# Kernel tuning notes

Hardware: AMD Instinct MI355X
Metric: run time of the kernel (lower is better)

The kernel has to match this reference:

```python
import jax, jax.numpy as jnp
import numpy as np

NH = 8  # num_heads


def _conv1x1(w, b, x):
    # 1x1 conv == channel matmul: w [O,C], x [B,C,H,W]
    return jnp.einsum('oc,bchw->bohw', w, x) + b[None, :, None, None]


def _fwd(low_freq_feat, high_freq_feat, ext_context, road_feat,
         ext_proj_w, ext_proj_b, road_proj_w, road_proj_b,
         ext_qkv_w, ext_qkv_b, road_qkv_w, road_qkv_b,
         ext_out_w, ext_out_b, road_out_w, road_out_b,
         gate_ext_w, gate_ext_b, gate_road_w, gate_road_b):
    B, C, H, W = low_freq_feat.shape
    nh = NH
    hd = C // nh
    HW = H * W
    scale = hd ** -0.5

    ext_p = ext_context @ ext_proj_w.T + ext_proj_b          # [B,C]
    road_p = _conv1x1(road_proj_w, road_proj_b, road_feat)   # [B,C,H,W]

    eqkv = (ext_p @ ext_qkv_w.T + ext_qkv_b).reshape(B, 3, nh, hd)
    ext_q, ext_v = eqkv[:, 0], eqkv[:, 2]                    # [B,nh,hd]

    # torch: conv out [B,3C,H,W] viewed as (B,C,3,H,W) -> q/k/v interleaved over channels
    rqkv = _conv1x1(road_qkv_w, road_qkv_b, road_p).reshape(B, C, 3, H, W)
    road_k = rqkv[:, :, 1].reshape(B, nh, hd, HW).transpose(0, 1, 3, 2)  # [B,nh,HW,hd]
    road_v = rqkv[:, :, 2].reshape(B, nh, hd, HW).transpose(0, 1, 3, 2)

    # ext->road attention. The torch code expands ext_q to HW identical rows; one row
    # per (batch, head) gives a bit-identical result without the [B,nh,HW,HW] blowup.
    scores = jnp.einsum('bnd,bnpd->bnp', ext_q, road_k) * scale
    attn = jax.nn.softmax(scores, axis=-1)                   # [B,nh,HW]
    ext_head = jnp.einsum('bnp,bnpd->bnd', attn, road_v).reshape(B, C)
    ext_vec = ext_head @ ext_out_w.T + ext_out_b             # [B,C]
    ext_feat_spatial = jnp.broadcast_to(ext_vec[:, :, None, None], (B, C, H, W))

    # road->ext attention: all HW keys/values are copies of the single ext token, so
    # softmax is exactly uniform and the output per position is exactly ext_v. The
    # road_out 1x1 conv on a spatially-constant map is a single matvec per batch.
    road_vec = ext_v.reshape(B, C) @ road_out_w.T + road_out_b
    road_enhanced = jnp.broadcast_to(road_vec[:, :, None, None], (B, C, H, W))

    # gated fusion (ext stream): spatial mean of constant map == ext_vec
    gate_in = jnp.concatenate([low_freq_feat.mean(axis=(2, 3)), ext_vec], axis=-1)
    ext_gate = jax.nn.sigmoid(gate_in @ gate_ext_w.T + gate_ext_b)[:, :, None, None]
    ext_final = low_freq_feat * (1.0 - ext_gate) + ext_feat_spatial * ext_gate

    # gated fusion (road stream)
    rg_in = jnp.concatenate([high_freq_feat, road_enhanced], axis=1)  # [B,2C,H,W]
    road_gate = jax.nn.sigmoid(_conv1x1(gate_road_w, gate_road_b, rg_in))
    road_final = high_freq_feat * (1.0 - road_gate) + road_enhanced * road_gate
    return ext_final, road_final


def setup_inputs() -> dict:
    key = jax.random.key(0)
    ks = jax.random.split(key, 20)
    B, C, H, W, E = 8, 256, 64, 64, 64
    f = lambda k, shape, s=1.0: jax.random.normal(k, shape, dtype=jnp.float32) * s
    return {
        'low_freq_feat': f(ks[0], (B, C, H, W)),
        'high_freq_feat': f(ks[1], (B, C, H, W)),
        'ext_context': f(ks[2], (B, E)),
        'road_feat': f(ks[3], (B, C, H, W)),
        'ext_proj_w': f(ks[4], (C, E), 0.05), 'ext_proj_b': f(ks[5], (C,), 0.02),
        'road_proj_w': f(ks[6], (C, C), 0.05), 'road_proj_b': f(ks[7], (C,), 0.02),
        'ext_qkv_w': f(ks[8], (3 * C, C), 0.05), 'ext_qkv_b': f(ks[9], (3 * C,), 0.02),
        'road_qkv_w': f(ks[10], (3 * C, C), 0.05), 'road_qkv_b': f(ks[11], (3 * C,), 0.02),
        'ext_out_w': f(ks[12], (C, C), 0.05), 'ext_out_b': f(ks[13], (C,), 0.02),
        'road_out_w': f(ks[14], (C, C), 0.05), 'road_out_b': f(ks[15], (C,), 0.02),
        'gate_ext_w': f(ks[16], (C, 2 * C), 0.05), 'gate_ext_b': f(ks[17], (C,), 0.02),
        'gate_road_w': f(ks[18], (C, 2 * C), 0.05), 'gate_road_b': f(ks[19], (C,), 0.02),
    }


def reference(low_freq_feat, high_freq_feat, ext_context, road_feat,
              ext_proj_w, ext_proj_b, road_proj_w, road_proj_b,
              ext_qkv_w, ext_qkv_b, road_qkv_w, road_qkv_b,
              ext_out_w, ext_out_b, road_out_w, road_out_b,
              gate_ext_w, gate_ext_b, gate_road_w, gate_road_b):
    return _fwd(low_freq_feat, high_freq_feat, ext_context, road_feat,
                ext_proj_w, ext_proj_b, road_proj_w, road_proj_b,
                ext_qkv_w, ext_qkv_b, road_qkv_w, road_qkv_b,
                ext_out_w, ext_out_b, road_out_w, road_out_b,
                gate_ext_w, gate_ext_b, gate_road_w, gate_road_b)
```

## Files before the change

### kernel.cpp

```cpp
#include <hip/hip_runtime.h>

typedef short bf16x8 __attribute__((ext_vector_type(8)));
typedef float f32x4 __attribute__((ext_vector_type(4)));

__device__ __forceinline__ unsigned short f2b(float f) {
    unsigned int u = __builtin_bit_cast(unsigned int, f);
    unsigned int r = u + 0x7FFFu + ((u >> 16) & 1u);
    return (unsigned short)(r >> 16);
}
__device__ __forceinline__ float wsum64(float v) {
    #pragma unroll
    for (int m = 32; m; m >>= 1) v += __shfl_xor(v, m, 64);
    return v;
}


__global__ __launch_bounds__(256) void k_setup(const float* __restrict__ w1,
                                               const float* __restrict__ wqkv,
                                               const float* __restrict__ b1,
                                               const float* __restrict__ bqkv,
                                               const float* __restrict__ gate_road_w,
                                               const float* __restrict__ ext_proj_w,
                                               const float* __restrict__ ext_qkv_w,
                                               const float* __restrict__ road_out_w,
                                               const float* __restrict__ ext_out_w,
                                               const float* __restrict__ gate_ext_w,
                                               const float* __restrict__ low,
                                               unsigned short* __restrict__ W3b,
                                               unsigned short* __restrict__ Wcb,
                                               unsigned short* __restrict__ WF,
                                               float* __restrict__ bcv,
                                               float* __restrict__ mean_low) {
    int bid = blockIdx.x, t = threadIdx.x;
    __shared__ float sel[8][256];
    __shared__ float red[8][4];
    if (bid >= 448) {
        int bc = bid - 448;
        const f32x4* p4 = (const f32x4*)(low + (size_t)bc * 4096);
        float s = 0.f;
        for (int i = t; i < 1024; i += 256) {
            f32x4 v = p4[i];
            s += v[0] + v[1] + v[2] + v[3];
        }
        s = wsum64(s);
        if ((t & 63) == 0) red[0][t >> 6] = s;
        __syncthreads();
        if (t == 0) mean_low[bc] = (red[0][0] + red[0][1] + red[0][2] + red[0][3]) * (1.0f / 4096.0f);
    } else if (bid < 256) {
        int i = bid * 256 + t;
        int o = i >> 8, k = i & 255;
        W3b[i] = f2b(gate_road_w[o * 512 + k]);
    } else if (bid < 320) {
        int o0 = (bid - 256) * 8;
        #pragma unroll
        for (int r = 0; r < 8; r++) {
            int o = o0 + r;
            int c = (o < 256) ? o : o - 256;
            int g = (o < 256) ? 1 : 2;
            sel[r][t] = wqkv[(size_t)(3 * c + g) * 256 + t];
        }
        __syncthreads();
        float b1v = b1[t];
        #pragma unroll
        for (int r = 0; r < 8; r++) {
            float v = wsum64(sel[r][t] * b1v);
            if ((t & 63) == 0) red[r][t >> 6] = v;
        }
        __syncthreads();
        if (t < 8) {
            int o = o0 + t;
            int c = (o < 256) ? o : o - 256;
            int g = (o < 256) ? 1 : 2;
            bcv[o] = red[t][0] + red[t][1] + red[t][2] + red[t][3] + bqkv[3 * c + g];
        }
        float acc[8] = {};
        #pragma unroll 16
        for (int m = 0; m < 256; m++) {
            float w1v = w1[(size_t)m * 256 + t];
            #pragma unroll
            for (int r = 0; r < 8; r++) acc[r] += sel[r][m] * w1v;
        }
        #pragma unroll
        for (int r = 0; r < 8; r++) Wcb[(size_t)(o0 + r) * 256 + t] = f2b(acc[r]);
    } else {
        int mb = bid - 320;
        int m = mb >> 4, ctile = mb & 15;
        const float* src;
        int stride, K, coff;
        unsigned short* dst;
        switch (m) {
        case 0: src = ext_qkv_w;                     stride = 256; K = 256; coff = 0;   dst = WF;          break;
        case 1: src = ext_qkv_w + (size_t)512 * 256; stride = 256; K = 256; coff = 0;   dst = WF + 65536;  break;
        case 2: src = road_out_w;                    stride = 256; K = 256; coff = 0;   dst = WF + 131072; break;
        case 3: src = gate_road_w;                   stride = 512; K = 256; coff = 256; dst = WF + 196608; break;
        case 4: src = ext_proj_w;                    stride = 64;  K = 64;  coff = 0;   dst = WF + 262144; break;
        case 5: src = ext_out_w;                     stride = 256; K = 256; coff = 0;   dst = WF + 278528; break;
        case 6: src = gate_ext_w;                    stride = 512; K = 256; coff = 0;   dst = WF + 344064; break;
        default: src = gate_ext_w;                   stride = 512; K = 256; coff = 256; dst = WF + 409600; break;
        }
        int lc = t >> 4, kseg = t & 15;
        int k0 = kseg * 16;
        if (k0 < K) {
            int c = ctile * 16 + lc;
            const float* sp = src + (size_t)c * stride + coff + k0;
            f32x4 v0 = *(const f32x4*)sp;
            f32x4 v1 = *(const f32x4*)(sp + 4);
            f32x4 v2 = *(const f32x4*)(sp + 8);
            f32x4 v3 = *(const f32x4*)(sp + 12);
            int kk = kseg >> 1;
            int Kt = K >> 5;
            #pragma unroll
            for (int h = 0; h < 2; h++) {
                int lhi = (kseg & 1) * 2 + h;
                int lane = lhi * 16 + lc;
                bf16x8 o;
                f32x4 a = h ? v2 : v0, b = h ? v3 : v1;
                #pragma unroll
                for (int i = 0; i < 4; i++) { o[i] = (short)f2b(a[i]); o[4 + i] = (short)f2b(b[i]); }
                *(bf16x8*)(dst + ((size_t)(ctile * Kt + kk) << 9) + lane * 8) = o;
            }
        }
    }
}

__global__ __launch_bounds__(256) void k_tiny(const unsigned short* __restrict__ WF,
                                              const float* __restrict__ ext_context,
                                              const float* __restrict__ ext_proj_b,
                                              const float* __restrict__ ext_qkv_b,
                                              const float* __restrict__ road_out_b,
                                              const float* __restrict__ gate_road_b,
                                              float* __restrict__ ext_q,
                                              float* __restrict__ road_vec,
                                              float* __restrict__ rg_const) {
    __shared__ unsigned short xA[16][264];
    __shared__ unsigned short xB[16][264];
    int t = threadIdx.x;
    int w = t >> 6, lane = t & 63, l15 = lane & 15, lhi = lane >> 4;
    const unsigned short* WqF  = WF;
    const unsigned short* WvF  = WF + 65536;
    const unsigned short* WroF = WF + 131072;
    const unsigned short* WgF  = WF + 196608;
    const unsigned short* WpF  = WF + 262144;
    {
        int b = t >> 5, k0 = (t & 31) * 2;
        float c0v = ext_context[b * 64 + k0];
        float c1v = ext_context[b * 64 + k0 + 1];
        *(unsigned int*)&xA[b][k0] = (unsigned int)f2b(c0v) | ((unsigned int)f2b(c1v) << 16);
    }
    __syncthreads();
    {
        f32x4 acc[4] = {};
        #pragma unroll
        for (int kk = 0; kk < 2; kk++) {
            bf16x8 a = *(const bf16x8*)&xA[l15][kk * 32 + 8 * lhi];
            #pragma unroll
            for (int ni = 0; ni < 4; ni++) {
                int ct = w * 4 + ni;
                bf16x8 bfr = *(const bf16x8*)(WpF + ((size_t)(ct * 2 + kk) << 9) + lane * 8);
                acc[ni] = __builtin_amdgcn_mfma_f32_16x16x32_bf16(a, bfr, acc[ni], 0, 0, 0);
            }
        }
        if (lhi < 2) {
            #pragma unroll
            for (int ni = 0; ni < 4; ni++) {
                int c = w * 64 + ni * 16 + l15;
                float bp = ext_proj_b[c];
                #pragma unroll
                for (int r = 0; r < 4; r++)
                    xB[4 * lhi + r][c] = f2b(acc[ni][r] + bp);
            }
        }
    }
    __syncthreads();
    {
        f32x4 acc[8] = {};
        bool isq = (w < 2);
        int cbase = (w & 1) * 128;
        const unsigned short* Wb = isq ? WqF : WvF;
        for (int kk = 0; kk < 8; kk++) {
            bf16x8 a = *(const bf16x8*)&xB[l15][kk * 32 + 8 * lhi];
            #pragma unroll
            for (int ni = 0; ni < 8; ni++) {
                int ct = (cbase >> 4) + ni;
                bf16x8 bfr = *(const bf16x8*)(Wb + ((size_t)(ct * 8 + kk) << 9) + lane * 8);
                acc[ni] = __builtin_amdgcn_mfma_f32_16x16x32_bf16(a, bfr, acc[ni], 0, 0, 0);
            }
        }
        if (lhi < 2) {
            #pragma unroll
            for (int ni = 0; ni < 8; ni++) {
                int c = cbase + ni * 16 + l15;
                float bb = ext_qkv_b[(isq ? 0 : 512) + c];
                #pragma unroll
                for (int r = 0; r < 4; r++) {
                    int b = 4 * lhi + r;
                    float val = acc[ni][r] + bb;
                    if (isq) ext_q[b * 256 + c] = val;
                    else     xA[b][c] = f2b(val);
                }
            }
        }
    }
    __syncthreads();
    {
        f32x4 acc[4] = {};
        for (int kk = 0; kk < 8; kk++) {
            bf16x8 a = *(const bf16x8*)&xA[l15][kk * 32 + 8 * lhi];
            #pragma unroll
            for (int ni = 0; ni < 4; ni++) {
                int ct = w * 4 + ni;
                bf16x8 bfr = *(const bf16x8*)(WroF + ((size_t)(ct * 8 + kk) << 9) + lane * 8);
                acc[ni] = __builtin_amdgcn_mfma_f32_16x16x32_bf16(a, bfr, acc[ni], 0, 0, 0);
            }
        }
        if (lhi < 2) {
            #pragma unroll
            for (int ni = 0; ni < 4; ni++) {
                int c = w * 64 + ni * 16 + l15;
                float bb = road_out_b[c];
                #pragma unroll
                for (int r = 0; r < 4; r++) {
                    int b = 4 * lhi + r;
                    float val = acc[ni][r] + bb;
                    road_vec[b * 256 + c] = val;
                    xB[b][c] = f2b(val);
                }
            }
        }
    }
    __syncthreads();
    {
        f32x4 acc[4] = {};
        for (int kk = 0; kk < 8; kk++) {
            bf16x8 a = *(const bf16x8*)&xB[l15][kk * 32 + 8 * lhi];
            #pragma unroll
            for (int ni = 0; ni < 4; ni++) {
                int ct = w * 4 + ni;
                bf16x8 bfr = *(const bf16x8*)(WgF + ((size_t)(ct * 8 + kk) << 9) + lane * 8);
                acc[ni] = __builtin_amdgcn_mfma_f32_16x16x32_bf16(a, bfr, acc[ni], 0, 0, 0);
            }
        }
        if (lhi < 2) {
            #pragma unroll
            for (int ni = 0; ni < 4; ni++) {
                int c = w * 64 + ni * 16 + l15;
                float bb = gate_road_b[c];
                #pragma unroll
                for (int r = 0; r < 4; r++)
                    rg_const[(4 * lhi + r) * 256 + c] = acc[ni][r] + bb;
            }
        }
    }
}

__global__ __launch_bounds__(512) void k_kv(const float* __restrict__ road_feat,
                                            const unsigned short* __restrict__ Wcb,
                                            const float* __restrict__ bcv,
                                            const float* __restrict__ extq,
                                            float* __restrict__ part) {
    __shared__ unsigned short Xs[32 * 256];
    __shared__ float esh[8][32];
    char* Xc = (char*)Xs;
    int bid = ((blockIdx.x & 7) << 7) | (blockIdx.x >> 3);
    int b  = bid >> 7;
    int p0 = (bid & 127) << 5;
    int t  = threadIdx.x;
    const float* rfb = road_feat + (size_t)b * 1048576;

    int c0 = 2 * (t >> 3);
    int j4 = (t & 7) * 4;
    #pragma unroll
    for (int it = 0; it < 2; ++it) {
        int c = c0 + 128 * it;
        f32x4 g0 = *(const f32x4*)(rfb + (size_t)c * 4096 + p0 + j4);
        f32x4 g1 = *(const f32x4*)(rfb + (size_t)(c + 1) * 4096 + p0 + j4);
        #pragma unroll
        for (int i = 0; i < 4; i++) {
            int j = j4 + i;
            unsigned int pk = (unsigned int)f2b(g0[i]) | ((unsigned int)f2b(g1[i]) << 16);
            *(unsigned int*)(Xc + ((j * 512 + 2 * c) ^ ((j & 15) << 4))) = pk;
        }
    }
    __syncthreads();

    int w = t >> 6, lane = t & 63, l15 = lane & 15, lhi = lane >> 4;

    f32x4 acc[2][4] = {};
    for (int kk = 0; kk < 8; kk++) {
        bf16x8 a[2];
        #pragma unroll
        for (int mi = 0; mi < 2; mi++) {
            int j = mi * 16 + l15;
            int off = (j * 512 + (kk * 32 + 8 * lhi) * 2) ^ ((j & 15) << 4);
            a[mi] = *(const bf16x8*)((const char*)Xs + off);
        }
        #pragma unroll
        for (int ni = 0; ni < 4; ni++) {
            int n = w * 64 + ni * 16 + l15;
            bf16x8 bf = *(const bf16x8*)(Wcb + (size_t)n * 256 + kk * 32 + 8 * lhi);
            acc[0][ni] = __builtin_amdgcn_mfma_f32_16x16x32_bf16(a[0], bf, acc[0][ni], 0, 0, 0);
            acc[1][ni] = __builtin_amdgcn_mfma_f32_16x16x32_bf16(a[1], bf, acc[1][ni], 0, 0, 0);
        }
    }

    if (w < 4) {
        float qv[4], bk[4];
        #pragma unroll
        for (int ni = 0; ni < 4; ni++) {
            int n = w * 64 + ni * 16 + l15;
            qv[ni] = extq[b * 256 + n];
            bk[ni] = bcv[n];
        }
        #pragma unroll
        for (int mi = 0; mi < 2; mi++)
            #pragma unroll
            for (int r = 0; r < 4; r++) {
                int j = mi * 16 + 4 * lhi + r;
                #pragma unroll
                for (int hl = 0; hl < 2; hl++) {
                    float s = (acc[mi][2 * hl][r] + bk[2 * hl]) * qv[2 * hl]
                            + (acc[mi][2 * hl + 1][r] + bk[2 * hl + 1]) * qv[2 * hl + 1];
                    s += __shfl_xor(s, 1, 64);
                    s += __shfl_xor(s, 2, 64);
                    s += __shfl_xor(s, 4, 64);
                    s += __shfl_xor(s, 8, 64);
                    if (l15 == 0)
                        esh[w * 2 + hl][j] = expf(s * 0.17677669529663687f);
                }
            }
    }
    __syncthreads();

    float* pb = part + (size_t)bid * 264;
    if (w >= 4) {
        #pragma unroll
        for (int ni = 0; ni < 4; ni++) {
            int cv = (w - 4) * 64 + ni * 16 + l15;
            int hg = (w - 4) * 2 + (ni >> 1);
            float bv = bcv[256 + cv];
            float p = 0.f;
            #pragma unroll
            for (int mi = 0; mi < 2; mi++)
                #pragma unroll
                for (int r = 0; r < 4; r++) {
                    int j = mi * 16 + 4 * lhi + r;
                    p += esh[hg][j] * (acc[mi][ni][r] + bv);
                }
            p += __shfl_xor(p, 16, 64);
            p += __shfl_xor(p, 32, 64);
            if (lhi == 0) pb[8 + cv] = p;
        }
    } else {
        int h0 = w * 2;
        float v0 = (lane < 32) ? esh[h0][lane] : esh[h0 + 1][lane - 32];
        v0 += __shfl_xor(v0, 1, 64);
        v0 += __shfl_xor(v0, 2, 64);
        v0 += __shfl_xor(v0, 4, 64);
        v0 += __shfl_xor(v0, 8, 64);
        v0 += __shfl_xor(v0, 16, 64);
        if (lane == 0)  pb[h0] = v0;
        if (lane == 32) pb[h0 + 1] = v0;
    }
}

__global__ __launch_bounds__(256) void k_vec_combine(const float* __restrict__ part,
                                                     float* __restrict__ hdg) {
    int b = blockIdx.x, c = threadIdx.x;
    __shared__ float tot[8];
    const float* pb = part + (size_t)b * 128 * 264;
    float a = 0.f;
    #pragma unroll 8
    for (int tile = 0; tile < 128; tile++) a += pb[tile * 264 + 8 + c];
    if (c < 8) {
        float s = 0.f;
        #pragma unroll 8
        for (int tile = 0; tile < 128; tile++) s += pb[tile * 264 + c];
        tot[c] = 1.0f / s;
    }
    __syncthreads();
    hdg[b * 256 + c] = a * tot[c >> 5];
}

__global__ __launch_bounds__(256) void k_vec2(const unsigned short* __restrict__ WF,
                                              const float* __restrict__ hdg,
                                              const float* __restrict__ mean_low,
                                              const float* __restrict__ ext_out_b,
                                              const float* __restrict__ gate_ext_b,
                                              float* __restrict__ ext_vec,
                                              float* __restrict__ ext_gate) {
    __shared__ unsigned short xA[16][264];
    __shared__ unsigned short xB[16][264];
    __shared__ unsigned short xC[16][264];
    int t = threadIdx.x;
    int w = t >> 6, lane = t & 63, l15 = lane & 15, lhi = lane >> 4;
    const unsigned short* WoF    = WF + 278528;
    const unsigned short* WgeLoF = WF + 344064;
    const unsigned short* WgeHiF = WF + 409600;
    {
        int bb = t >> 5, kb = t & 31;
        #pragma unroll
        for (int q = 0; q < 4; q++) {
            int k0 = (kb + 32 * q) * 2;
            *(unsigned int*)&xA[bb][k0] =
                (unsigned int)f2b(hdg[bb * 256 + k0]) | ((unsigned int)f2b(hdg[bb * 256 + k0 + 1]) << 16);
            *(unsigned int*)&xB[bb][k0] =
                (unsigned int)f2b(mean_low[bb * 256 + k0]) | ((unsigned int)f2b(mean_low[bb * 256 + k0 + 1]) << 16);
        }
    }
    __syncthreads();
    {
        f32x4 acc[4] = {};
        for (int kk = 0; kk < 8; kk++) {
            bf16x8 a = *(const bf16x8*)&xA[l15][kk * 32 + 8 * lhi];
            #pragma unroll
            for (int ni = 0; ni < 4; ni++) {
                int ct = w * 4 + ni;
                bf16x8 bfr = *(const bf16x8*)(WoF + ((size_t)(ct * 8 + kk) << 9) + lane * 8);
                acc[ni] = __builtin_amdgcn_mfma_f32_16x16x32_bf16(a, bfr, acc[ni], 0, 0, 0);
            }
        }
        if (lhi < 2) {
            #pragma unroll
            for (int ni = 0; ni < 4; ni++) {
                int c = w * 64 + ni * 16 + l15;
                float bb = ext_out_b[c];
                #pragma unroll
                for (int r = 0; r < 4; r++) {
                    int b = 4 * lhi + r;
                    float val = acc[ni][r] + bb;
                    ext_vec[b * 256 + c] = val;
                    xC[b][c] = f2b(val);
                }
            }
        }
    }
    __syncthreads();
    {
        f32x4 acc[4] = {};
        for (int kk = 0; kk < 8; kk++) {
            bf16x8 a = *(const bf16x8*)&xB[l15][kk * 32 + 8 * lhi];
            #pragma unroll
            for (int ni = 0; ni < 4; ni++) {
                int ct = w * 4 + ni;
                bf16x8 bfr = *(const bf16x8*)(WgeLoF + ((size_t)(ct * 8 + kk) << 9) + lane * 8);
                acc[ni] = __builtin_amdgcn_mfma_f32_16x16x32_bf16(a, bfr, acc[ni], 0, 0, 0);
            }
        }
        for (int kk = 0; kk < 8; kk++) {
            bf16x8 a = *(const bf16x8*)&xC[l15][kk * 32 + 8 * lhi];
            #pragma unroll
            for (int ni = 0; ni < 4; ni++) {
                int ct = w * 4 + ni;
                bf16x8 bfr = *(const bf16x8*)(WgeHiF + ((size_t)(ct * 8 + kk) << 9) + lane * 8);
                acc[ni] = __builtin_amdgcn_mfma_f32_16x16x32_bf16(a, bfr, acc[ni], 0, 0, 0);
            }
        }
        if (lhi < 2) {
            #pragma unroll
            for (int ni = 0; ni < 4; ni++) {
                int c = w * 64 + ni * 16 + l15;
                float bb = gate_ext_b[c];
                #pragma unroll
                for (int r = 0; r < 4; r++) {
                    int b = 4 * lhi + r;
                    ext_gate[b * 256 + c] = 1.0f / (1.0f + expf(-(acc[ni][r] + bb)));
                }
            }
        }
    }
}

__global__ __launch_bounds__(256) void k_ext_final(const float* __restrict__ low,
                                                   const float* __restrict__ ext_vec,
                                                   const float* __restrict__ ext_gate,
                                                   float* __restrict__ out) {
    int idx = blockIdx.x * 256 + threadIdx.x;
    #pragma unroll
    for (int rep = 0; rep < 4; ++rep) {
        int i = idx + rep * 524288;
        int bc = i >> 10;
        float g = ext_gate[bc];
        float vv = ext_vec[bc];
        f32x4 L = *(const f32x4*)(low + (size_t)i * 4);
        f32x4 o;
        #pragma unroll
        for (int c = 0; c < 4; c++) o[c] = L[c] + g * (vv - L[c]);
        *(f32x4*)(out + (size_t)i * 4) = o;
    }
}

__global__ __launch_bounds__(512) void k_road(const float* __restrict__ high,
                                              const unsigned short* __restrict__ W3b,
                                              const float* __restrict__ rg_const,
                                              const float* __restrict__ road_vec,
                                              float* __restrict__ outbuf) {
    __shared__ float Xs[32 * 256];
    char* Xc = (char*)Xs;
    int bid = ((blockIdx.x & 7) << 7) | (blockIdx.x >> 3);
    int b  = bid >> 7;
    int p0 = (bid & 127) << 5;
    int t  = threadIdx.x;
    const float* hb = high + (size_t)b * 1048576;

    int c0 = t >> 3;
    int j4 = (t & 7) * 4;
    #pragma unroll
    for (int it = 0; it < 4; ++it) {
        int c = c0 + 64 * it;
        f32x4 g = *(const f32x4*)(hb + (size_t)c * 4096 + p0 + j4);
        #pragma unroll
        for (int i = 0; i < 4; i++) {
            int j = j4 + i;
            *(float*)(Xc + ((j * 1024 + 4 * c) ^ ((j & 15) << 4))) = g[i];
        }
    }
    __syncthreads();

    int w = t >> 6, lane = t & 63, l15 = lane & 15, lhi = lane >> 4;
    f32x4 acc[2][2] = {};
    for (int kk = 0; kk < 8; kk++) {
        bf16x8 a[2];
        #pragma unroll
        for (int mi = 0; mi < 2; mi++) {
            int j = mi * 16 + l15;
            int base = j * 1024 + (kk * 32 + 8 * lhi) * 4;
            int sw = (j & 15) << 4;
            f32x4 x0 = *(const f32x4*)(Xc + (base ^ sw));
            f32x4 x1 = *(const f32x4*)(Xc + ((base + 16) ^ sw));
            bf16x8 av;
            #pragma unroll
            for (int i = 0; i < 4; i++) {
                av[i]     = (short)f2b(x0[i]);
                av[4 + i] = (short)f2b(x1[i]);
            }
            a[mi] = av;
        }
        #pragma unroll
        for (int ni = 0; ni < 2; ni++) {
            int o = w * 32 + ni * 16 + l15;
            bf16x8 bf = *(const bf16x8*)(W3b + (size_t)o * 256 + kk * 32 + 8 * lhi);
            acc[0][ni] = __builtin_amdgcn_mfma_f32_16x16x32_bf16(a[0], bf, acc[0][ni], 0, 0, 0);
            acc[1][ni] = __builtin_amdgcn_mfma_f32_16x16x32_bf16(a[1], bf, acc[1][ni], 0, 0, 0);
        }
    }
    __syncthreads();

    #pragma unroll
    for (int ni = 0; ni < 2; ni++) {
        int o = w * 32 + ni * 16 + l15;
        float rc = rg_const[b * 256 + o];
        float rv = road_vec[b * 256 + o];
        #pragma unroll
        for (int mi = 0; mi < 2; mi++)
            #pragma unroll
            for (int r = 0; r < 4; r++) {
                int j = mi * 16 + 4 * lhi + r;
                float* slot = (float*)(Xc + ((j * 1024 + 4 * o) ^ ((j & 15) << 4)));
                float z = acc[mi][ni][r] + rc;
                float gte = 1.0f / (1.0f + expf(-z));
                float hv = *slot;
                *slot = hv + gte * (rv - hv);
            }
    }
    __syncthreads();

    float* ob = outbuf + 8388608 + (size_t)b * 1048576;
    #pragma unroll
    for (int it = 0; it < 4; ++it) {
        int c = c0 + 64 * it;
        f32x4 o4;
        #pragma unroll
        for (int i = 0; i < 4; i++) {
            int j = j4 + i;
            o4[i] = *(const float*)(Xc + ((j * 1024 + 4 * c) ^ ((j & 15) << 4)));
        }
        *(f32x4*)(ob + (size_t)c * 4096 + p0 + j4) = o4;
    }
}

extern "C" void kernel_launch(void* const* d_in, const int* in_sizes, int n_in,
                              void* d_out, int out_size, void* d_ws, size_t ws_size,
                              hipStream_t stream) {
    const float* low         = (const float*)d_in[0];
    const float* high        = (const float*)d_in[1];
    const float* ext_context = (const float*)d_in[2];
    const float* road_feat   = (const float*)d_in[3];
    const float* ext_proj_w  = (const float*)d_in[4];
    const float* ext_proj_b  = (const float*)d_in[5];
    const float* road_proj_w = (const float*)d_in[6];
    const float* road_proj_b = (const float*)d_in[7];
    const float* ext_qkv_w   = (const float*)d_in[8];
    const float* ext_qkv_b   = (const float*)d_in[9];
    const float* road_qkv_w  = (const float*)d_in[10];
    const float* road_qkv_b  = (const float*)d_in[11];
    const float* ext_out_w   = (const float*)d_in[12];
    const float* ext_out_b   = (const float*)d_in[13];
    const float* road_out_w  = (const float*)d_in[14];
    const float* road_out_b  = (const float*)d_in[15];
    const float* gate_ext_w  = (const float*)d_in[16];
    const float* gate_ext_b  = (const float*)d_in[17];
    const float* gate_road_w = (const float*)d_in[18];
    const float* gate_road_b = (const float*)d_in[19];

    float* out = (float*)d_out;
    unsigned short* wsb = (unsigned short*)d_ws;
    unsigned short* Wcb = wsb;
    unsigned short* W3b = wsb + 131072;
    float* fw = (float*)((char*)d_ws + 983040);
    float* ext_q    = fw;
    float* road_vec = fw + 2048;
    float* rg_const = fw + 4096;
    float* ext_vec  = fw + 8192;
    float* ext_gate = fw + 10240;
    float* mean_low = fw + 12288;
    float* bcv      = fw + 14336;
    float* hdg      = fw + 16384;
    float* part = out + 2097152;
    unsigned short* WF = (unsigned short*)(out + 4194304);

    k_setup<<<2496, 256, 0, stream>>>(road_proj_w, road_qkv_w, road_proj_b, road_qkv_b,
                                      gate_road_w, ext_proj_w, ext_qkv_w, road_out_w,
                                      ext_out_w, gate_ext_w, low,
                                      W3b, Wcb, WF, bcv, mean_low);
    k_tiny<<<1, 256, 0, stream>>>(WF, ext_context, ext_proj_b, ext_qkv_b,
                                  road_out_b, gate_road_b, ext_q, road_vec, rg_const);
    k_kv<<<1024, 512, 0, stream>>>(road_feat, Wcb, bcv, ext_q, part);
    k_vec_combine<<<8, 256, 0, stream>>>(part, hdg);
    k_vec2<<<1, 256, 0, stream>>>(WF, hdg, mean_low, ext_out_b, gate_ext_b,
                                  ext_vec, ext_gate);
    k_ext_final<<<2048, 256, 0, stream>>>(low, ext_vec, ext_gate, out);
    k_road<<<1024, 512, 0, stream>>>(high, W3b, rg_const, road_vec, out);
}
```

Baseline: 156.1 us.

## Assign per-head K and V columns to each wave to drop block barrier

```diff
diff --git a/kernel.cpp b/kernel.cpp
--- a/kernel.cpp
+++ b/kernel.cpp
@@ -261,7 +261,7 @@
     __shared__ unsigned short Xs[32 * 256];
     __shared__ float esh[8][32];
     char* Xc = (char*)Xs;
-    int bid = ((blockIdx.x & 7) << 7) | (blockIdx.x >> 3);
+    int bid = blockIdx.x;
     int b  = bid >> 7;
     int p0 = (bid & 127) << 5;
     int t  = threadIdx.x;
@@ -296,70 +296,56 @@
         }
         #pragma unroll
         for (int ni = 0; ni < 4; ni++) {
-            int n = w * 64 + ni * 16 + l15;
+            int n = (ni < 2) ? (w * 32 + ni * 16 + l15) : (256 + w * 32 + (ni - 2) * 16 + l15);
             bf16x8 bf = *(const bf16x8*)(Wcb + (size_t)n * 256 + kk * 32 + 8 * lhi);
             acc[0][ni] = __builtin_amdgcn_mfma_f32_16x16x32_bf16(a[0], bf, acc[0][ni], 0, 0, 0);
             acc[1][ni] = __builtin_amdgcn_mfma_f32_16x16x32_bf16(a[1], bf, acc[1][ni], 0, 0, 0);
         }
     }
 
-    if (w < 4) {
-        float qv[4], bk[4];
-        #pragma unroll
-        for (int ni = 0; ni < 4; ni++) {
-            int n = w * 64 + ni * 16 + l15;
-            qv[ni] = extq[b * 256 + n];
-            bk[ni] = bcv[n];
-        }
-        #pragma unroll
-        for (int mi = 0; mi < 2; mi++)
-            #pragma unroll
-            for (int r = 0; r < 4; r++) {
-                int j = mi * 16 + 4 * lhi + r;
-                #pragma unroll
-                for (int hl = 0; hl < 2; hl++) {
-                    float s = (acc[mi][2 * hl][r] + bk[2 * hl]) * qv[2 * hl]
-                            + (acc[mi][2 * hl + 1][r] + bk[2 * hl + 1]) * qv[2 * hl + 1];
-                    s += __shfl_xor(s, 1, 64);
-                    s += __shfl_xor(s, 2, 64);
-                    s += __shfl_xor(s, 4, 64);
-                    s += __shfl_xor(s, 8, 64);
-                    if (l15 == 0)
-                        esh[w * 2 + hl][j] = expf(s * 0.17677669529663687f);
-                }
-            }
-    }
-    __syncthreads();
+    float q0 = extq[b * 256 + w * 32 + l15];
+    float q1 = extq[b * 256 + w * 32 + 16 + l15];
+    float bk0 = bcv[w * 32 + l15];
+    float bk1 = bcv[w * 32 + 16 + l15];
+    #pragma unroll
+    for (int mi = 0; mi < 2; mi++)
+        #pragma unroll
+        for (int r = 0; r < 4; r++) {
+            int j = mi * 16 + 4 * lhi + r;
+            float s = (acc[mi][0][r] + bk0) * q0 + (acc[mi][1][r] + bk1) * q1;
+            s += __shfl_xor(s, 1, 64);
+            s += __shfl_xor(s, 2, 64);
+            s += __shfl_xor(s, 4, 64);
+            s += __shfl_xor(s, 8, 64);
+            if (l15 == 0)
+                esh[w][j] = expf(s * 0.17677669529663687f);
+        }
 
     float* pb = part + (size_t)bid * 264;
-    if (w >= 4) {
-        #pragma unroll
-        for (int ni = 0; ni < 4; ni++) {
-            int cv = (w - 4) * 64 + ni * 16 + l15;
-            int hg = (w - 4) * 2 + (ni >> 1);
-            float bv = bcv[256 + cv];
-            float p = 0.f;
-            #pragma unroll
-            for (int mi = 0; mi < 2; mi++)
-                #pragma unroll
-                for (int r = 0; r < 4; r++) {
-                    int j = mi * 16 + 4 * lhi + r;
-                    p += esh[hg][j] * (acc[mi][ni][r] + bv);
-                }
-            p += __shfl_xor(p, 16, 64);
-            p += __shfl_xor(p, 32, 64);
-            if (lhi == 0) pb[8 + cv] = p;
-        }
-    } else {
-        int h0 = w * 2;
-        float v0 = (lane < 32) ? esh[h0][lane] : esh[h0 + 1][lane - 32];
+    {
+        float v0 = esh[w][lane & 31];
         v0 += __shfl_xor(v0, 1, 64);
         v0 += __shfl_xor(v0, 2, 64);
         v0 += __shfl_xor(v0, 4, 64);
         v0 += __shfl_xor(v0, 8, 64);
         v0 += __shfl_xor(v0, 16, 64);
-        if (lane == 0)  pb[h0] = v0;
-        if (lane == 32) pb[h0 + 1] = v0;
+        if (lane == 0) pb[w] = v0;
+    }
+    #pragma unroll
+    for (int vi = 0; vi < 2; vi++) {
+        int cv = w * 32 + vi * 16 + l15;
+        float bv = bcv[256 + cv];
+        float p = 0.f;
+        #pragma unroll
+        for (int mi = 0; mi < 2; mi++)
+            #pragma unroll
+            for (int r = 0; r < 4; r++) {
+                int j = mi * 16 + 4 * lhi + r;
+                p += esh[w][j] * (acc[mi][2 + vi][r] + bv);
+            }
+        p += __shfl_xor(p, 16, 64);
+        p += __shfl_xor(p, 32, 64);
+        if (lhi == 0) pb[8 + cv] = p;
     }
 }
 
@@ -496,7 +482,7 @@
                                               float* __restrict__ outbuf) {
     __shared__ float Xs[32 * 256];
     char* Xc = (char*)Xs;
-    int bid = ((blockIdx.x & 7) << 7) | (blockIdx.x >> 3);
+    int bid = blockIdx.x;
     int b  = bid >> 7;
     int p0 = (bid & 127) << 5;
     int t  = threadIdx.x;
```

Measured after the change: 156.0 us. About the same (-0.1%).
